# Kernel optimization log

Hardware: AMD Instinct MI355X
Metric: run time of the kernel (lower is better)

Reference implementation:

```python
import jax, jax.numpy as jnp
import numpy as np

B, S, H, W, L = 16, 2048, 512, 4, 2  # batch, seq, projection_dim, width, n_layers
EPS = 1e-5


def _ln(x, g, b):
    m = jnp.mean(x, axis=-1, keepdims=True)
    v = jnp.mean((x - m) ** 2, axis=-1, keepdims=True)
    return g * (x - m) * jax.lax.rsqrt(v + EPS) + b


def setup_inputs() -> dict:
    key = jax.random.key(0)
    ks = jax.random.split(key, 24)
    s = 0.02
    d = {
        'inputs': jax.random.normal(ks[0], (B, S, H), jnp.float32),
        'left_padding': jax.random.normal(ks[1], (W, H), jnp.float32) * s,
        'right_padding': jax.random.normal(ks[2], (W, H), jnp.float32) * s,
        'Wl': jax.random.normal(ks[3], (W * H, H), jnp.float32) * s,
        'bl': jnp.zeros((H,), jnp.float32),
        'Wr': jax.random.normal(ks[4], (W * H, H), jnp.float32) * s,
        'br': jnp.zeros((H,), jnp.float32),
        'lw1': jax.random.normal(ks[5], (L, H, H), jnp.float32) * s,
        'lb1': jnp.zeros((L, H), jnp.float32),
        'lw2': jax.random.normal(ks[6], (L, H, H), jnp.float32) * s,
        'lb2': jnp.zeros((L, H), jnp.float32),
        'lg': jnp.ones((L, H), jnp.float32),
        'lbeta': jnp.zeros((L, H), jnp.float32),
        'rw1': jax.random.normal(ks[7], (L, H, H), jnp.float32) * s,
        'rb1': jnp.zeros((L, H), jnp.float32),
        'rw2': jax.random.normal(ks[8], (L, H, H), jnp.float32) * s,
        'rb2': jnp.zeros((L, H), jnp.float32),
        'rg': jnp.ones((L, H), jnp.float32),
        'rbeta': jnp.zeros((L, H), jnp.float32),
    }
    return d


def reference(inputs, left_padding, right_padding, Wl, bl, Wr, br,
              lw1, lb1, lw2, lb2, lg, lbeta,
              rw1, rb1, rw2, rb2, rg, rbeta):
    b, s, h = inputs.shape
    w = left_padding.shape[0]
    padded = jnp.concatenate([
        jnp.broadcast_to(left_padding, (b, w, h)), inputs,
        jnp.broadcast_to(right_padding, (b, w, h))], axis=1)  # [B, W+S+W, H]
    t = jnp.arange(s)[:, None]
    off = jnp.arange(w)[None, :]
    left = padded[:, t + off].reshape(b, s, w * h)           # rows [t, t+w)
    right = padded[:, t + (w + 1) + off].reshape(b, s, w * h)  # rows [t+w+1, t+2w+1)
    lo = jax.nn.relu(jnp.einsum('bsk,kh->bsh', left, Wl) + bl)
    ro = jax.nn.relu(jnp.einsum('bsk,kh->bsh', right, Wr) + br)
    layers = []
    for i in range(lw1.shape[0]):
        # SublayerConnection: x + FF(LayerNorm(x)); FF = w2(relu(w1(.)))
        lo = lo + jnp.einsum('bsh,hk->bsk', jax.nn.relu(
            jnp.einsum('bsh,hk->bsk', _ln(lo, lg[i], lbeta[i]), lw1[i]) + lb1[i]), lw2[i]) + lb2[i]
        ro = ro + jnp.einsum('bsh,hk->bsk', jax.nn.relu(
            jnp.einsum('bsh,hk->bsk', _ln(ro, rg[i], rbeta[i]), rw1[i]) + rb1[i]), rw2[i]) + rb2[i]
        layers.append(jnp.concatenate([lo, ro], axis=-1))  # [B,S,2H]
    stacked = jnp.stack(layers, axis=0)                 # [L,B,S,2H]
    all_layers = jnp.transpose(stacked, (0, 2, 1, 3))   # [L,S,B,2H]
    last_layers = layers[-1]                            # [B,S,2H]
    return all_layers, last_layers
```

## Files before the change

### kernel.cpp

```cpp
#include <hip/hip_runtime.h>
#include <stdint.h>

#define Bx   16
#define Sx   2048
#define Hx   512
#define Lx   2
#define PHx  2056
#define Mx   32768

typedef float f32x4  __attribute__((ext_vector_type(4)));
typedef __bf16 bf16x8 __attribute__((ext_vector_type(8)));
typedef unsigned short u16x8 __attribute__((ext_vector_type(8)));

typedef __attribute__((address_space(1))) void gvoid_t;
typedef __attribute__((address_space(3))) void lvoid_t;

__device__ __forceinline__ unsigned short f2bf(float f) {
  uint32_t u = __float_as_uint(f);
  u += 0x7FFFu + ((u >> 16) & 1u);
  return (unsigned short)(u >> 16);
}

__global__ __launch_bounds__(256) void build_padded_k(
    const float* __restrict__ inp, const float* __restrict__ lp,
    const float* __restrict__ rp, unsigned short* __restrict__ padded) {
  int64_t idx = ((int64_t)blockIdx.x * 256 + threadIdx.x) * 8;
  int h = (int)(idx & 511);
  int64_t rowi = idx >> 9;
  int r = (int)(rowi % 2056);
  int b = (int)(rowi / 2056);
  const float* src;
  if (r < 4)          src = lp + r * 512 + h;
  else if (r < 2052)  src = inp + ((int64_t)b * 2048 + (r - 4)) * 512 + h;
  else                src = rp + (r - 2052) * 512 + h;
  float4 u = ((const float4*)src)[0];
  float4 w = ((const float4*)src)[1];
  u16x8 o;
  o[0] = f2bf(u.x); o[1] = f2bf(u.y); o[2] = f2bf(u.z); o[3] = f2bf(u.w);
  o[4] = f2bf(w.x); o[5] = f2bf(w.y); o[6] = f2bf(w.z); o[7] = f2bf(w.w);
  *(u16x8*)(padded + idx) = o;
}

__global__ __launch_bounds__(256) void prep_weights_k(
    const float* __restrict__ Wl, const float* __restrict__ Wr,
    const float* __restrict__ lw1, const float* __restrict__ lw2,
    const float* __restrict__ rw1, const float* __restrict__ rw2,
    unsigned short* __restrict__ Wlt, unsigned short* __restrict__ Wrt,
    unsigned short* __restrict__ lw1t, unsigned short* __restrict__ lw2t,
    unsigned short* __restrict__ rw1t, unsigned short* __restrict__ rw2t) {
  __shared__ unsigned short tl[32][36];
  int b = blockIdx.x;
  const float* src; unsigned short* dst; int K, tk, tn;
  if (b < 2048) {
    src = (b < 1024) ? Wl : Wr;
    dst = (b < 1024) ? Wlt : Wrt;
    int t = b & 1023; tk = t >> 4; tn = t & 15; K = 2048;
  } else {
    int b2 = b - 2048;
    int mat = b2 >> 8;
    const float* srcs[8] = {lw1, lw1 + 262144, lw2, lw2 + 262144,
                            rw1, rw1 + 262144, rw2, rw2 + 262144};
    unsigned short* dsts[8] = {lw1t, lw1t + 262144, lw2t, lw2t + 262144,
                               rw1t, rw1t + 262144, rw2t, rw2t + 262144};
    src = srcs[mat]; dst = dsts[mat];
    int tt = b2 & 255; tk = tt >> 4; tn = tt & 15; K = 512;
  }
  int t = threadIdx.x;
  int rr = t >> 3, c4 = (t & 7) * 4;
  float4 v = *(const float4*)(src + (int64_t)(tk * 32 + rr) * 512 + tn * 32 + c4);
  tl[c4 + 0][rr] = f2bf(v.x);
  tl[c4 + 1][rr] = f2bf(v.y);
  tl[c4 + 2][rr] = f2bf(v.z);
  tl[c4 + 3][rr] = f2bf(v.w);
  __syncthreads();
  int nn = t >> 3, k4 = (t & 7) * 4;
  ushort4 o = {tl[nn][k4], tl[nn][k4 + 1], tl[nn][k4 + 2], tl[nn][k4 + 3]};
  *(ushort4*)(dst + (int64_t)(tn * 32 + nn) * K + tk * 32 + k4) = o;
}

template <int MODE, bool STATS>
__global__ __launch_bounds__(256) void gemm_k(
    const unsigned short* __restrict__ A0, const unsigned short* __restrict__ A1,
    int64_t a_bstride, int a_off_per_z, int K,
    const unsigned short* __restrict__ Bt0, const unsigned short* __restrict__ Bt1,
    const float* __restrict__ bias0, const float* __restrict__ bias1,
    float* __restrict__ C, float* __restrict__ out0p, float* __restrict__ P) {
  __shared__ unsigned short sA[128 * 32];
  __shared__ unsigned short sB[128 * 32];
  __shared__ float sls[128][2][2];
  const int tid  = threadIdx.x;
  const int lane = tid & 63;
  const int wave = tid >> 6;
  const int m0 = blockIdx.x * 128;
  const int n0 = blockIdx.y * 128;
  const int z  = blockIdx.z;
  const int wm = (wave >> 1) * 64;
  const int wn = (wave & 1) * 64;
  const int fr = lane >> 4;
  const int fc = lane & 15;

  const unsigned short* A  = z ? A1 : A0;
  const unsigned short* Bt = z ? Bt1 : Bt0;
  const float* bias = z ? bias1 : bias0;
  const int a_off = z * a_off_per_z;
  const int c_off = z * 512;

  const unsigned short* Ablk =
      A + (int64_t)(m0 >> 11) * a_bstride + (int64_t)(m0 & 2047) * 512 + a_off;
  const unsigned short* Bblk = Bt + (int64_t)n0 * K;

  f32x4 acc[4][4] = {};

  const int t0 = tid, t1 = tid + 256;
  const int ar0 = t0 >> 2, ac0 = (t0 & 3) * 8;
  const int ar1 = t1 >> 2, ac1 = (t1 & 3) * 8;

  for (int k0 = 0; k0 < K; k0 += 32) {
    __builtin_amdgcn_global_load_lds(
        (gvoid_t*)(Ablk + (int64_t)ar0 * 512 + k0 + ac0),
        (lvoid_t*)(sA + t0 * 8), 16, 0, 0);
    __builtin_amdgcn_global_load_lds(
        (gvoid_t*)(Ablk + (int64_t)ar1 * 512 + k0 + ac1),
        (lvoid_t*)(sA + t1 * 8), 16, 0, 0);
    __builtin_amdgcn_global_load_lds(
        (gvoid_t*)(Bblk + (int64_t)ar0 * K + k0 + ac0),
        (lvoid_t*)(sB + t0 * 8), 16, 0, 0);
    __builtin_amdgcn_global_load_lds(
        (gvoid_t*)(Bblk + (int64_t)ar1 * K + k0 + ac1),
        (lvoid_t*)(sB + t1 * 8), 16, 0, 0);
    __syncthreads();

    bf16x8 af[4], bf[4];
#pragma unroll
    for (int i = 0; i < 4; i++)
      af[i] = *(const bf16x8*)(sA + (wm + i * 16 + fc) * 32 + fr * 8);
#pragma unroll
    for (int j = 0; j < 4; j++)
      bf[j] = *(const bf16x8*)(sB + (wn + j * 16 + fc) * 32 + fr * 8);
#pragma unroll
    for (int i = 0; i < 4; i++)
#pragma unroll
      for (int j = 0; j < 4; j++)
        acc[i][j] = __builtin_amdgcn_mfma_f32_16x16x32_bf16(af[i], bf[j], acc[i][j], 0, 0, 0);
    __syncthreads();
  }

  int col[4];
  float bv[4];
#pragma unroll
  for (int j = 0; j < 4; j++) {
    col[j] = n0 + wn + j * 16 + fc;
    bv[j] = bias[col[j]];
  }
  const int b_idx = m0 >> 11;
#pragma unroll
  for (int i = 0; i < 4; i++) {
#pragma unroll
    for (int r = 0; r < 4; r++) {
      const int m = m0 + wm + i * 16 + fr * 4 + r;
      const int64_t base = (int64_t)m * 1024 + c_off;
      float vs[4];
      if (MODE == 0) {
#pragma unroll
        for (int j = 0; j < 4; j++) {
          float v = acc[i][j][r] + bv[j];
          v = v > 0.f ? v : 0.f;
          C[base + col[j]] = v;
          vs[j] = v;
        }
      } else {
        const int s = m & 2047;
        const int64_t obase = (int64_t)s * 16384 + (int64_t)b_idx * 1024 + c_off;
#pragma unroll
        for (int j = 0; j < 4; j++) {
          float v = C[base + col[j]] + acc[i][j][r] + bv[j];
          C[base + col[j]] = v;
          out0p[obase + col[j]] = v;
          vs[j] = v;
        }
      }
      if (STATS) {
        float s1 = vs[0] + vs[1] + vs[2] + vs[3];
        float s2 = vs[0] * vs[0] + vs[1] * vs[1] + vs[2] * vs[2] + vs[3] * vs[3];
#pragma unroll
        for (int o = 1; o < 16; o <<= 1) {
          s1 += __shfl_xor(s1, o);
          s2 += __shfl_xor(s2, o);
        }
        if (fc == 0) {
          int li = (wave >> 1) * 64 + i * 16 + fr * 4 + r;
          sls[li][wave & 1][0] = s1;
          sls[li][wave & 1][1] = s2;
        }
      }
    }
  }
  if (STATS) {
    __syncthreads();
    int li = tid >> 1, comp = tid & 1;
    float v = sls[li][0][comp] + sls[li][1][comp];
    P[(((int64_t)z * 4 + blockIdx.y) * Mx + m0 + li) * 2 + comp] = v;
  }
}

__global__ __launch_bounds__(256) void gemm_ln_k(
    const float* __restrict__ state, const float* __restrict__ P,
    const float* __restrict__ g0, const float* __restrict__ g1p,
    const float* __restrict__ be0, const float* __restrict__ be1,
    const unsigned short* __restrict__ Bt0, const unsigned short* __restrict__ Bt1,
    const float* __restrict__ bias0, const float* __restrict__ bias1,
    unsigned short* __restrict__ hidden) {
  __shared__ unsigned short sA[128 * 32];
  __shared__ unsigned short sB[128 * 32];
  const int tid  = threadIdx.x;
  const int lane = tid & 63;
  const int wave = tid >> 6;
  const int m0 = blockIdx.x * 128;
  const int n0 = blockIdx.y * 128;
  const int z  = blockIdx.z;
  const int wm = (wave >> 1) * 64;
  const int wn = (wave & 1) * 64;
  const int fr = lane >> 4;
  const int fc = lane & 15;

  const unsigned short* Bt = z ? Bt1 : Bt0;
  const float* bias = z ? bias1 : bias0;
  const float* g    = z ? g1p : g0;
  const float* be   = z ? be1 : be0;
  const int c_off = z * 512;
  const unsigned short* Bblk = Bt + (int64_t)n0 * 512;

  const int row  = tid >> 1;
  const int half = tid & 1;
  const int m = m0 + row;
  const float* srcrow = state + (int64_t)m * 1024 + c_off + half * 16;

  float s1 = 0.f, s2 = 0.f;
#pragma unroll
  for (int nb = 0; nb < 4; nb++) {
    s1 += P[(((int64_t)z * 4 + nb) * Mx + m) * 2 + 0];
    s2 += P[(((int64_t)z * 4 + nb) * Mx + m) * 2 + 1];
  }
  const float mean = s1 * (1.0f / 512.0f);
  const float rstd = rsqrtf(s2 * (1.0f / 512.0f) - mean * mean + 1e-5f);

  f32x4 acc[4][4] = {};

  const int t0 = tid, t1 = tid + 256;
  const int br0 = t0 >> 2, bc0 = (t0 & 3) * 8;
  const int br1 = t1 >> 2, bc1 = (t1 & 3) * 8;

  for (int k0 = 0; k0 < 512; k0 += 32) {
    __builtin_amdgcn_global_load_lds(
        (gvoid_t*)(Bblk + (int64_t)br0 * 512 + k0 + bc0),
        (lvoid_t*)(sB + t0 * 8), 16, 0, 0);
    __builtin_amdgcn_global_load_lds(
        (gvoid_t*)(Bblk + (int64_t)br1 * 512 + k0 + bc1),
        (lvoid_t*)(sB + t1 * 8), 16, 0, 0);

    const float* sp = srcrow + k0;
    float xs[16], gs[16], bs[16];
    *(float4*)(xs + 0)  = ((const float4*)sp)[0];
    *(float4*)(xs + 4)  = ((const float4*)sp)[1];
    *(float4*)(xs + 8)  = ((const float4*)sp)[2];
    *(float4*)(xs + 12) = ((const float4*)sp)[3];
    const float* gp = g + k0 + half * 16;
    const float* bp = be + k0 + half * 16;
    *(float4*)(gs + 0)  = ((const float4*)gp)[0];
    *(float4*)(gs + 4)  = ((const float4*)gp)[1];
    *(float4*)(gs + 8)  = ((const float4*)gp)[2];
    *(float4*)(gs + 12) = ((const float4*)gp)[3];
    *(float4*)(bs + 0)  = ((const float4*)bp)[0];
    *(float4*)(bs + 4)  = ((const float4*)bp)[1];
    *(float4*)(bs + 8)  = ((const float4*)bp)[2];
    *(float4*)(bs + 12) = ((const float4*)bp)[3];
    u16x8 o0, o1;
#pragma unroll
    for (int t = 0; t < 8; t++)
      o0[t] = f2bf((xs[t] - mean) * rstd * gs[t] + bs[t]);
#pragma unroll
    for (int t = 0; t < 8; t++)
      o1[t] = f2bf((xs[t + 8] - mean) * rstd * gs[t + 8] + bs[t + 8]);
    *(u16x8*)(sA + row * 32 + half * 16)     = o0;
    *(u16x8*)(sA + row * 32 + half * 16 + 8) = o1;
    __syncthreads();

    bf16x8 af[4], bf[4];
#pragma unroll
    for (int i = 0; i < 4; i++)
      af[i] = *(const bf16x8*)(sA + (wm + i * 16 + fc) * 32 + fr * 8);
#pragma unroll
    for (int j = 0; j < 4; j++)
      bf[j] = *(const bf16x8*)(sB + (wn + j * 16 + fc) * 32 + fr * 8);
#pragma unroll
    for (int i = 0; i < 4; i++)
#pragma unroll
      for (int j = 0; j < 4; j++)
        acc[i][j] = __builtin_amdgcn_mfma_f32_16x16x32_bf16(af[i], bf[j], acc[i][j], 0, 0, 0);
    __syncthreads();
  }

  unsigned short* Cb = hidden + (int64_t)z * Mx * 512;
  int col[4];
  float bv[4];
#pragma unroll
  for (int j = 0; j < 4; j++) {
    col[j] = n0 + wn + j * 16 + fc;
    bv[j] = bias[col[j]];
  }
#pragma unroll
  for (int i = 0; i < 4; i++) {
#pragma unroll
    for (int r = 0; r < 4; r++) {
      const int mm = m0 + wm + i * 16 + fr * 4 + r;
      const int64_t base = (int64_t)mm * 512;
#pragma unroll
      for (int j = 0; j < 4; j++) {
        float v = acc[i][j][r] + bv[j];
        Cb[base + col[j]] = f2bf(v > 0.f ? v : 0.f);
      }
    }
  }
}

extern "C" void kernel_launch(void* const* d_in, const int* in_sizes, int n_in,
                              void* d_out, int out_size, void* d_ws, size_t ws_size,
                              hipStream_t stream) {
  const float* inputs = (const float*)d_in[0];
  const float* lp     = (const float*)d_in[1];
  const float* rp     = (const float*)d_in[2];
  const float* Wl     = (const float*)d_in[3];
  const float* bl     = (const float*)d_in[4];
  const float* Wr     = (const float*)d_in[5];
  const float* br     = (const float*)d_in[6];
  const float* lw1    = (const float*)d_in[7];
  const float* lb1    = (const float*)d_in[8];
  const float* lw2    = (const float*)d_in[9];
  const float* lb2    = (const float*)d_in[10];
  const float* lg     = (const float*)d_in[11];
  const float* lbeta  = (const float*)d_in[12];
  const float* rw1    = (const float*)d_in[13];
  const float* rb1    = (const float*)d_in[14];
  const float* rw2    = (const float*)d_in[15];
  const float* rb2    = (const float*)d_in[16];
  const float* rg     = (const float*)d_in[17];
  const float* rbeta  = (const float*)d_in[18];

  float* out0 = (float*)d_out;
  float* out1 = out0 + (int64_t)Lx * Sx * Bx * 1024;

  char* w = (char*)d_ws;
  auto take = [&](size_t n) { char* p = w; w += (n + 255) & ~(size_t)255; return p; };
  unsigned short* padded = (unsigned short*)take((size_t)Bx * PHx * Hx * 2);
  unsigned short* Wlt    = (unsigned short*)take(2048ull * 512 * 2);
  unsigned short* Wrt    = (unsigned short*)take(2048ull * 512 * 2);
  unsigned short* lw1t   = (unsigned short*)take((size_t)Lx * 512 * 512 * 2);
  unsigned short* lw2t   = (unsigned short*)take((size_t)Lx * 512 * 512 * 2);
  unsigned short* rw1t   = (unsigned short*)take((size_t)Lx * 512 * 512 * 2);
  unsigned short* rw2t   = (unsigned short*)take((size_t)Lx * 512 * 512 * 2);
  unsigned short* hidden = (unsigned short*)take((size_t)2 * Mx * 512 * 2);
  float*          Pst    = (float*)take((size_t)2 * 4 * Mx * 2 * 4);

  build_padded_k<<<8224, 256, 0, stream>>>(inputs, lp, rp, padded);
  prep_weights_k<<<4096, 256, 0, stream>>>(Wl, Wr, lw1, lw2, rw1, rw2,
                                           Wlt, Wrt, lw1t, lw2t, rw1t, rw2t);

  dim3 gg(256, 4, 2);
  gemm_k<0, true><<<gg, 256, 0, stream>>>(
      padded, padded, (int64_t)PHx * 512, 5 * 512, 2048,
      Wlt, Wrt, bl, br, out1, nullptr, Pst);

  for (int i = 0; i < Lx; i++) {
    gemm_ln_k<<<gg, 256, 0, stream>>>(
        out1, Pst, lg + i * 512, rg + i * 512, lbeta + i * 512, rbeta + i * 512,
        lw1t + (int64_t)i * 262144, rw1t + (int64_t)i * 262144,
        lb1 + i * 512, rb1 + i * 512, hidden);
    if (i == 0) {
      gemm_k<2, true><<<gg, 256, 0, stream>>>(
          hidden, hidden + (int64_t)Mx * 512, (int64_t)2048 * 512, 0, 512,
          lw2t, rw2t, lb2, rb2, out1, out0, Pst);
    } else {
      gemm_k<2, false><<<gg, 256, 0, stream>>>(
          hidden, hidden + (int64_t)Mx * 512, (int64_t)2048 * 512, 0, 512,
          lw2t + (int64_t)i * 262144, rw2t + (int64_t)i * 262144,
          lb2 + i * 512, rb2 + i * 512, out1,
          out0 + (int64_t)i * Sx * Bx * 1024, nullptr);
    }
  }
}
```

Baseline: 1.079 ms.

## Double K-tile depth to 64 and XOR-swizzle LDS layout in GEMM kernels

Both GEMM kernels now stage 64-wide K slices per iteration instead of 32, halving the number of barrier pairs per K loop. The LDS layout uses an XOR swizzle on 8-element chunks (applied on the global-load source address and on fragment reads) to avoid bank conflicts with the wider 128-byte rows. LDS use per block doubles, which may reduce occupancy.

```diff
diff --git a/kernel.cpp b/kernel.cpp
--- a/kernel.cpp
+++ b/kernel.cpp
@@ -20,6 +20,7 @@
   u += 0x7FFFu + ((u >> 16) & 1u);
   return (unsigned short)(u >> 16);
 }
+
 
 __global__ __launch_bounds__(256) void build_padded_k(
     const float* __restrict__ inp, const float* __restrict__ lp,
@@ -85,8 +86,8 @@
     const unsigned short* __restrict__ Bt0, const unsigned short* __restrict__ Bt1,
     const float* __restrict__ bias0, const float* __restrict__ bias1,
     float* __restrict__ C, float* __restrict__ out0p, float* __restrict__ P) {
-  __shared__ unsigned short sA[128 * 32];
-  __shared__ unsigned short sB[128 * 32];
+  __shared__ unsigned short sA[128 * 64];
+  __shared__ unsigned short sB[128 * 64];
   __shared__ float sls[128][2][2];
   const int tid  = threadIdx.x;
   const int lane = tid & 63;
@@ -98,6 +99,7 @@
   const int wn = (wave & 1) * 64;
   const int fr = lane >> 4;
   const int fc = lane & 15;
+  const int swf = (fc & 7) << 3;
 
   const unsigned short* A  = z ? A1 : A0;
   const unsigned short* Bt = z ? Bt1 : Bt0;
@@ -111,37 +113,37 @@
 
   f32x4 acc[4][4] = {};
 
-  const int t0 = tid, t1 = tid + 256;
-  const int ar0 = t0 >> 2, ac0 = (t0 & 3) * 8;
-  const int ar1 = t1 >> 2, ac1 = (t1 & 3) * 8;
-
-  for (int k0 = 0; k0 < K; k0 += 32) {
-    __builtin_amdgcn_global_load_lds(
-        (gvoid_t*)(Ablk + (int64_t)ar0 * 512 + k0 + ac0),
-        (lvoid_t*)(sA + t0 * 8), 16, 0, 0);
-    __builtin_amdgcn_global_load_lds(
-        (gvoid_t*)(Ablk + (int64_t)ar1 * 512 + k0 + ac1),
-        (lvoid_t*)(sA + t1 * 8), 16, 0, 0);
-    __builtin_amdgcn_global_load_lds(
-        (gvoid_t*)(Bblk + (int64_t)ar0 * K + k0 + ac0),
-        (lvoid_t*)(sB + t0 * 8), 16, 0, 0);
-    __builtin_amdgcn_global_load_lds(
-        (gvoid_t*)(Bblk + (int64_t)ar1 * K + k0 + ac1),
-        (lvoid_t*)(sB + t1 * 8), 16, 0, 0);
+  for (int k0 = 0; k0 < K; k0 += 64) {
+#pragma unroll
+    for (int r = 0; r < 4; r++) {
+      const int tt = tid + r * 256;
+      const int ar = tt >> 3;
+      const int ac = (tt & 7) * 8;
+      const int acs = ac ^ ((ar & 7) << 3);
+      __builtin_amdgcn_global_load_lds(
+          (gvoid_t*)(Ablk + (int64_t)ar * 512 + k0 + acs),
+          (lvoid_t*)(sA + tt * 8), 16, 0, 0);
+      __builtin_amdgcn_global_load_lds(
+          (gvoid_t*)(Bblk + (int64_t)ar * K + k0 + acs),
+          (lvoid_t*)(sB + tt * 8), 16, 0, 0);
+    }
     __syncthreads();
 
-    bf16x8 af[4], bf[4];
-#pragma unroll
-    for (int i = 0; i < 4; i++)
-      af[i] = *(const bf16x8*)(sA + (wm + i * 16 + fc) * 32 + fr * 8);
-#pragma unroll
-    for (int j = 0; j < 4; j++)
-      bf[j] = *(const bf16x8*)(sB + (wn + j * 16 + fc) * 32 + fr * 8);
-#pragma unroll
-    for (int i = 0; i < 4; i++)
+#pragma unroll
+    for (int kk = 0; kk < 2; kk++) {
+      bf16x8 af[4], bf[4];
+#pragma unroll
+      for (int i = 0; i < 4; i++)
+        af[i] = *(const bf16x8*)(sA + (((wm + i * 16 + fc) * 64 + kk * 32 + fr * 8) ^ swf));
 #pragma unroll
       for (int j = 0; j < 4; j++)
-        acc[i][j] = __builtin_amdgcn_mfma_f32_16x16x32_bf16(af[i], bf[j], acc[i][j], 0, 0, 0);
+        bf[j] = *(const bf16x8*)(sB + (((wn + j * 16 + fc) * 64 + kk * 32 + fr * 8) ^ swf));
+#pragma unroll
+      for (int i = 0; i < 4; i++)
+#pragma unroll
+        for (int j = 0; j < 4; j++)
+          acc[i][j] = __builtin_amdgcn_mfma_f32_16x16x32_bf16(af[i], bf[j], acc[i][j], 0, 0, 0);
+    }
     __syncthreads();
   }
 
@@ -210,8 +212,8 @@
     const unsigned short* __restrict__ Bt0, const unsigned short* __restrict__ Bt1,
     const float* __restrict__ bias0, const float* __restrict__ bias1,
     unsigned short* __restrict__ hidden) {
-  __shared__ unsigned short sA[128 * 32];
-  __shared__ unsigned short sB[128 * 32];
+  __shared__ unsigned short sA[128 * 64];
+  __shared__ unsigned short sB[128 * 64];
   const int tid  = threadIdx.x;
   const int lane = tid & 63;
   const int wave = tid >> 6;
@@ -222,6 +224,7 @@
   const int wn = (wave & 1) * 64;
   const int fr = lane >> 4;
   const int fc = lane & 15;
+  const int swf = (fc & 7) << 3;
 
   const unsigned short* Bt = z ? Bt1 : Bt0;
   const float* bias = z ? bias1 : bias0;
@@ -233,7 +236,8 @@
   const int row  = tid >> 1;
   const int half = tid & 1;
   const int m = m0 + row;
-  const float* srcrow = state + (int64_t)m * 1024 + c_off + half * 16;
+  const int swr = (row & 7) << 3;
+  const float* srcrow = state + (int64_t)m * 1024 + c_off;
 
   float s1 = 0.f, s2 = 0.f;
 #pragma unroll
@@ -246,57 +250,64 @@
 
   f32x4 acc[4][4] = {};
 
-  const int t0 = tid, t1 = tid + 256;
-  const int br0 = t0 >> 2, bc0 = (t0 & 3) * 8;
-  const int br1 = t1 >> 2, bc1 = (t1 & 3) * 8;
-
-  for (int k0 = 0; k0 < 512; k0 += 32) {
-    __builtin_amdgcn_global_load_lds(
-        (gvoid_t*)(Bblk + (int64_t)br0 * 512 + k0 + bc0),
-        (lvoid_t*)(sB + t0 * 8), 16, 0, 0);
-    __builtin_amdgcn_global_load_lds(
-        (gvoid_t*)(Bblk + (int64_t)br1 * 512 + k0 + bc1),
-        (lvoid_t*)(sB + t1 * 8), 16, 0, 0);
-
-    const float* sp = srcrow + k0;
-    float xs[16], gs[16], bs[16];
-    *(float4*)(xs + 0)  = ((const float4*)sp)[0];
-    *(float4*)(xs + 4)  = ((const float4*)sp)[1];
-    *(float4*)(xs + 8)  = ((const float4*)sp)[2];
-    *(float4*)(xs + 12) = ((const float4*)sp)[3];
-    const float* gp = g + k0 + half * 16;
-    const float* bp = be + k0 + half * 16;
-    *(float4*)(gs + 0)  = ((const float4*)gp)[0];
-    *(float4*)(gs + 4)  = ((const float4*)gp)[1];
-    *(float4*)(gs + 8)  = ((const float4*)gp)[2];
-    *(float4*)(gs + 12) = ((const float4*)gp)[3];
-    *(float4*)(bs + 0)  = ((const float4*)bp)[0];
-    *(float4*)(bs + 4)  = ((const float4*)bp)[1];
-    *(float4*)(bs + 8)  = ((const float4*)bp)[2];
-    *(float4*)(bs + 12) = ((const float4*)bp)[3];
-    u16x8 o0, o1;
-#pragma unroll
-    for (int t = 0; t < 8; t++)
-      o0[t] = f2bf((xs[t] - mean) * rstd * gs[t] + bs[t]);
-#pragma unroll
-    for (int t = 0; t < 8; t++)
-      o1[t] = f2bf((xs[t + 8] - mean) * rstd * gs[t + 8] + bs[t + 8]);
-    *(u16x8*)(sA + row * 32 + half * 16)     = o0;
-    *(u16x8*)(sA + row * 32 + half * 16 + 8) = o1;
+  for (int k0 = 0; k0 < 512; k0 += 64) {
+#pragma unroll
+    for (int r = 0; r < 4; r++) {
+      const int tt = tid + r * 256;
+      const int br = tt >> 3;
+      const int bc = (tt & 7) * 8;
+      const int bcs = bc ^ ((br & 7) << 3);
+      __builtin_amdgcn_global_load_lds(
+          (gvoid_t*)(Bblk + (int64_t)br * 512 + k0 + bcs),
+          (lvoid_t*)(sB + tt * 8), 16, 0, 0);
+    }
+
+#pragma unroll
+    for (int sc = 0; sc < 2; sc++) {
+      const int cb = half * 32 + sc * 16;
+      const float* xp = srcrow + k0 + cb;
+      const float* gp = g + k0 + cb;
+      const float* bp = be + k0 + cb;
+      float xs[16], gs[16], bs[16];
+      *(float4*)(xs + 0)  = ((const float4*)xp)[0];
+      *(float4*)(xs + 4)  = ((const float4*)xp)[1];
+      *(float4*)(xs + 8)  = ((const float4*)xp)[2];
+      *(float4*)(xs + 12) = ((const float4*)xp)[3];
+      *(float4*)(gs + 0)  = ((const float4*)gp)[0];
+      *(float4*)(gs + 4)  = ((const float4*)gp)[1];
+      *(float4*)(gs + 8)  = ((const float4*)gp)[2];
+      *(float4*)(gs + 12) = ((const float4*)gp)[3];
+      *(float4*)(bs + 0)  = ((const float4*)bp)[0];
+      *(float4*)(bs + 4)  = ((const float4*)bp)[1];
+      *(float4*)(bs + 8)  = ((const float4*)bp)[2];
+      *(float4*)(bs + 12) = ((const float4*)bp)[3];
+      u16x8 o0, o1;
+#pragma unroll
+      for (int t = 0; t < 8; t++)
+        o0[t] = f2bf((xs[t] - mean) * rstd * gs[t] + bs[t]);
+#pragma unroll
+      for (int t = 0; t < 8; t++)
+        o1[t] = f2bf((xs[t + 8] - mean) * rstd * gs[t + 8] + bs[t + 8]);
+      *(u16x8*)(sA + ((row * 64 + cb) ^ swr))     = o0;
+      *(u16x8*)(sA + ((row * 64 + cb + 8) ^ swr)) = o1;
+    }
     __syncthreads();
 
-    bf16x8 af[4], bf[4];
-#pragma unroll
-    for (int i = 0; i < 4; i++)
-      af[i] = *(const bf16x8*)(sA + (wm + i * 16 + fc) * 32 + fr * 8);
-#pragma unroll
-    for (int j = 0; j < 4; j++)
-      bf[j] = *(const bf16x8*)(sB + (wn + j * 16 + fc) * 32 + fr * 8);
-#pragma unroll
-    for (int i = 0; i < 4; i++)
+#pragma unroll
+    for (int kk = 0; kk < 2; kk++) {
+      bf16x8 af[4], bf[4];
+#pragma unroll
+      for (int i = 0; i < 4; i++)
+        af[i] = *(const bf16x8*)(sA + (((wm + i * 16 + fc) * 64 + kk * 32 + fr * 8) ^ swf));
 #pragma unroll
       for (int j = 0; j < 4; j++)
-        acc[i][j] = __builtin_amdgcn_mfma_f32_16x16x32_bf16(af[i], bf[j], acc[i][j], 0, 0, 0);
+        bf[j] = *(const bf16x8*)(sB + (((wn + j * 16 + fc) * 64 + kk * 32 + fr * 8) ^ swf));
+#pragma unroll
+      for (int i = 0; i < 4; i++)
+#pragma unroll
+        for (int j = 0; j < 4; j++)
+          acc[i][j] = __builtin_amdgcn_mfma_f32_16x16x32_bf16(af[i], bf[j], acc[i][j], 0, 0, 0);
+    }
     __syncthreads();
   }
 
```

After: 1.171 ms. 1.09x slower.

## Add 256x256-tile pipelined projection GEMM kernel with direct-to-LDS loads

Applied to the files above, without the earlier changes.

Replaces the generic 128x128 gemm_k used for the initial windowed projection (K=2048) with a dedicated 512-thread kernel. Each block computes a 256x256 output tile. The kernel uses global_load_lds async copies into eight swizzled LDS slots and hand-scheduled vmcnt waits and barriers, so loads overlap with MFMA work. It also raises wave priority around the MFMA bursts. The larger tile improves data reuse and cuts global traffic for the dominant GEMM, at the cost of 128KB of LDS, heavy register pressure and fragile manual scheduling.

```diff
diff --git a/kernel.cpp b/kernel.cpp
--- a/kernel.cpp
+++ b/kernel.cpp
@@ -20,6 +20,17 @@
   u += 0x7FFFu + ((u >> 16) & 1u);
   return (unsigned short)(u >> 16);
 }
+
+__device__ __forceinline__ void sbar() {
+  __builtin_amdgcn_sched_barrier(0);
+  __builtin_amdgcn_s_barrier();
+  __builtin_amdgcn_sched_barrier(0);
+}
+#define VMCNT(n) do {                                        \
+    __builtin_amdgcn_sched_barrier(0);                       \
+    asm volatile("s_waitcnt vmcnt(" #n ")" ::: "memory");    \
+    __builtin_amdgcn_sched_barrier(0);                       \
+  } while (0)
 
 __global__ __launch_bounds__(256) void build_padded_k(
     const float* __restrict__ inp, const float* __restrict__ lp,
@@ -78,6 +89,170 @@
   *(ushort4*)(dst + (int64_t)(tn * 32 + nn) * K + tk * 32 + k4) = o;
 }
 
+__global__ __launch_bounds__(512, 2) void proj8_k(
+    const unsigned short* __restrict__ A,
+    const unsigned short* __restrict__ Bt0, const unsigned short* __restrict__ Bt1,
+    const float* __restrict__ bias0, const float* __restrict__ bias1,
+    float* __restrict__ C, float* __restrict__ P) {
+  __shared__ unsigned short lds[8][8192];
+  const int tid  = threadIdx.x;
+  const int lane = tid & 63;
+  const int wave = tid >> 6;
+  const int wy = wave >> 2;
+  const int wx = wave & 3;
+  const int fr = lane >> 4;
+  const int fc = lane & 15;
+  const int m0   = blockIdx.x * 256;
+  const int nblk = blockIdx.y;
+  const int z    = blockIdx.z;
+
+  const unsigned short* Bt = z ? Bt1 : Bt0;
+  const float* bias = z ? bias1 : bias0;
+  const unsigned short* Ablk = A + (int64_t)(m0 >> 11) * ((int64_t)PHx * 512)
+                                 + (int64_t)(m0 & 2047) * 512 + z * 2560;
+  const unsigned short* Bblk = Bt + (int64_t)nblk * 256 * 2048;
+
+  auto stage = [&](int slot, int isB, int h, int tile) {
+#pragma unroll
+    for (int L = 0; L < 2; ++L) {
+      const int tt = tid + L * 512;
+      const int row = tt >> 3;
+      const int chunk = (tt & 7) * 8;
+      const int scol = chunk ^ (((row >> 2) & 1) << 4);
+      const unsigned short* src = isB
+          ? Bblk + (int64_t)(h * 128 + row) * 2048 + tile * 64 + scol
+          : Ablk + (int64_t)(h * 128 + row) * 512  + tile * 64 + scol;
+      __builtin_amdgcn_global_load_lds((gvoid_t*)src,
+          (lvoid_t*)(&lds[slot][tt * 8]), 16, 0, 0);
+    }
+  };
+  auto rdA = [&](int buf, int h, int i, int kk) -> bf16x8 {
+    const int row = wy * 64 + i * 16 + fc;
+    const int e = (row * 64 + kk * 32 + fr * 8) ^ (((row >> 2) & 1) << 4);
+    return *(const bf16x8*)(&lds[buf * 4 + h][e]);
+  };
+  auto rdB = [&](int buf, int h, int j, int kk) -> bf16x8 {
+    const int row = wx * 32 + j * 16 + fc;
+    const int e = (row * 64 + kk * 32 + fr * 8) ^ (((row >> 2) & 1) << 4);
+    return *(const bf16x8*)(&lds[buf * 4 + 2 + h][e]);
+  };
+
+  f32x4 acc[4][4][2] = {};
+
+  stage(0, 0, 0, 0);
+  stage(2, 1, 0, 0);
+  stage(1, 0, 1, 0);
+  stage(3, 1, 1, 0);
+  stage(4, 0, 0, 1);
+  stage(6, 1, 0, 1);
+  VMCNT(4);
+  sbar();
+
+  for (int t = 0; t < 16; ++t) {
+    const int t2 = 2 * t;
+    const bool notlast = (t < 15);
+#pragma unroll
+    for (int hv = 0; hv < 2; ++hv) {
+      const int buf = hv;
+#pragma unroll
+      for (int pp = 0; pp < 4; ++pp) {
+        const int mq = pp >> 1, nq = pp & 1;
+        bf16x8 af[4][2], bv[2][2];
+#pragma unroll
+        for (int i = 0; i < 4; ++i)
+#pragma unroll
+          for (int kk = 0; kk < 2; ++kk) af[i][kk] = rdA(buf, mq, i, kk);
+#pragma unroll
+        for (int j = 0; j < 2; ++j)
+#pragma unroll
+          for (int kk = 0; kk < 2; ++kk) bv[j][kk] = rdB(buf, nq, j, kk);
+
+        const int p = hv * 4 + pp;
+        if (p == 0)        stage(5, 0, 1, t2 + 1);
+        else if (p == 1)   stage(7, 1, 1, t2 + 1);
+        else if (notlast) {
+          if (p == 2)      stage(0, 0, 0, t2 + 2);
+          else if (p == 3) stage(2, 1, 0, t2 + 2);
+          else if (p == 4) stage(1, 0, 1, t2 + 2);
+          else if (p == 5) stage(3, 1, 1, t2 + 2);
+          else if (p == 6) stage(4, 0, 0, t2 + 3);
+          else             stage(6, 1, 0, t2 + 3);
+        }
+        sbar();
+        __builtin_amdgcn_s_setprio(1);
+#pragma unroll
+        for (int i = 0; i < 4; ++i)
+#pragma unroll
+          for (int j = 0; j < 2; ++j)
+#pragma unroll
+            for (int kk = 0; kk < 2; ++kk)
+              acc[pp][i][j] = __builtin_amdgcn_mfma_f32_16x16x32_bf16(
+                  af[i][kk], bv[j][kk], acc[pp][i][j], 0, 0, 0);
+        __builtin_amdgcn_s_setprio(0);
+        if (pp == 3) {
+          if (hv == 0) {
+            if (notlast) { VMCNT(4); } else { VMCNT(0); }
+          } else {
+            if (notlast) { VMCNT(4); }
+          }
+        }
+        sbar();
+      }
+    }
+  }
+
+  __syncthreads();
+
+  float* sls = (float*)&lds[0][0];
+  float bvv[2][2];
+#pragma unroll
+  for (int nq = 0; nq < 2; ++nq)
+#pragma unroll
+    for (int j = 0; j < 2; ++j)
+      bvv[nq][j] = bias[nblk * 256 + nq * 128 + wx * 32 + j * 16 + fc];
+
+#pragma unroll
+  for (int q = 0; q < 4; ++q) {
+    const int mq = q >> 1, nq = q & 1;
+#pragma unroll
+    for (int i = 0; i < 4; ++i) {
+#pragma unroll
+      for (int r = 0; r < 4; ++r) {
+        const int row_l = mq * 128 + wy * 64 + i * 16 + fr * 4 + r;
+        const int m = m0 + row_l;
+        float v0 = acc[q][i][0][r] + bvv[nq][0]; v0 = v0 > 0.f ? v0 : 0.f;
+        float v1 = acc[q][i][1][r] + bvv[nq][1]; v1 = v1 > 0.f ? v1 : 0.f;
+        const int64_t cb = (int64_t)m * 1024 + z * 512
+                           + nblk * 256 + nq * 128 + wx * 32 + fc;
+        C[cb] = v0;
+        C[cb + 16] = v1;
+        float s1 = v0 + v1, s2 = v0 * v0 + v1 * v1;
+#pragma unroll
+        for (int o = 1; o < 16; o <<= 1) {
+          s1 += __shfl_xor(s1, o);
+          s2 += __shfl_xor(s2, o);
+        }
+        if (fc == 0) {
+          sls[(row_l * 4 + wx) * 4 + nq * 2 + 0] = s1;
+          sls[(row_l * 4 + wx) * 4 + nq * 2 + 1] = s2;
+        }
+      }
+    }
+  }
+  __syncthreads();
+  {
+    const int row = tid >> 1, comp = tid & 1;
+#pragma unroll
+    for (int nq = 0; nq < 2; ++nq) {
+      float v = 0.f;
+#pragma unroll
+      for (int wxx = 0; wxx < 4; ++wxx)
+        v += sls[(row * 4 + wxx) * 4 + nq * 2 + comp];
+      P[(((int64_t)z * 4 + nblk * 2 + nq) * Mx + m0 + row) * 2 + comp] = v;
+    }
+  }
+}
+
 template <int MODE, bool STATS>
 __global__ __launch_bounds__(256) void gemm_k(
     const unsigned short* __restrict__ A0, const unsigned short* __restrict__ A1,
@@ -365,22 +540,20 @@
   prep_weights_k<<<4096, 256, 0, stream>>>(Wl, Wr, lw1, lw2, rw1, rw2,
                                            Wlt, Wrt, lw1t, lw2t, rw1t, rw2t);
 
-  dim3 gg(256, 4, 2);
-  gemm_k<0, true><<<gg, 256, 0, stream>>>(
-      padded, padded, (int64_t)PHx * 512, 5 * 512, 2048,
-      Wlt, Wrt, bl, br, out1, nullptr, Pst);
+  proj8_k<<<dim3(128, 2, 2), 512, 0, stream>>>(
+      padded, Wlt, Wrt, bl, br, out1, Pst);
 
   for (int i = 0; i < Lx; i++) {
-    gemm_ln_k<<<gg, 256, 0, stream>>>(
+    gemm_ln_k<<<dim3(256, 4, 2), 256, 0, stream>>>(
         out1, Pst, lg + i * 512, rg + i * 512, lbeta + i * 512, rbeta + i * 512,
         lw1t + (int64_t)i * 262144, rw1t + (int64_t)i * 262144,
         lb1 + i * 512, rb1 + i * 512, hidden);
     if (i == 0) {
-      gemm_k<2, true><<<gg, 256, 0, stream>>>(
+      gemm_k<2, true><<<dim3(256, 4, 2), 256, 0, stream>>>(
           hidden, hidden + (int64_t)Mx * 512, (int64_t)2048 * 512, 0, 512,
           lw2t, rw2t, lb2, rb2, out1, out0, Pst);
     } else {
-      gemm_k<2, false><<<gg, 256, 0, stream>>>(
+      gemm_k<2, false><<<dim3(256, 4, 2), 256, 0, stream>>>(
           hidden, hidden + (int64_t)Mx * 512, (int64_t)2048 * 512, 0, 512,
           lw2t + (int64_t)i * 262144, rw2t + (int64_t)i * 262144,
           lb2 + i * 512, rb2 + i * 512, out1,
```

Measured after the change: 1.080 ms. Within noise of the previous version (+0.1%).

## Double-buffer LDS tiles with XOR swizzle and enlarge gemm_k tile to 256 rows

Applied to the files above, without the earlier changes.

Both GEMM kernels now prefetch the next K-slice into a second LDS buffer while the current one feeds the MFMAs, which removes one barrier per iteration and overlaps global loads with compute. LDS column groups are XOR-swizzled by row to reduce bank conflicts on fragment reads. gemm_k moves to 512 threads with a 256x128 tile and half as many blocks, giving more reuse of B per block. The cost is more LDS per block and fewer blocks, which can lower occupancy.

```diff
diff --git a/kernel.cpp b/kernel.cpp
--- a/kernel.cpp
+++ b/kernel.cpp
@@ -20,6 +20,7 @@
   u += 0x7FFFu + ((u >> 16) & 1u);
   return (unsigned short)(u >> 16);
 }
+
 
 __global__ __launch_bounds__(256) void build_padded_k(
     const float* __restrict__ inp, const float* __restrict__ lp,
@@ -79,15 +80,148 @@
 }
 
 template <int MODE, bool STATS>
-__global__ __launch_bounds__(256) void gemm_k(
+__global__ __launch_bounds__(512) void gemm_k(
     const unsigned short* __restrict__ A0, const unsigned short* __restrict__ A1,
     int64_t a_bstride, int a_off_per_z, int K,
     const unsigned short* __restrict__ Bt0, const unsigned short* __restrict__ Bt1,
     const float* __restrict__ bias0, const float* __restrict__ bias1,
     float* __restrict__ C, float* __restrict__ out0p, float* __restrict__ P) {
-  __shared__ unsigned short sA[128 * 32];
-  __shared__ unsigned short sB[128 * 32];
-  __shared__ float sls[128][2][2];
+  __shared__ unsigned short sA[2][256 * 32];
+  __shared__ unsigned short sB[2][128 * 32];
+  __shared__ float sls[256][2][2];
+  const int tid  = threadIdx.x;
+  const int lane = tid & 63;
+  const int wave = tid >> 6;
+  const int m0 = blockIdx.x * 256;
+  const int n0 = blockIdx.y * 128;
+  const int z  = blockIdx.z;
+  const int wm = (wave >> 1) * 64;
+  const int wn = (wave & 1) * 64;
+  const int fr = lane >> 4;
+  const int fc = lane & 15;
+  const int swA = ((fr ^ (fc & 3)) << 3);
+
+  const unsigned short* A  = z ? A1 : A0;
+  const unsigned short* Bt = z ? Bt1 : Bt0;
+  const float* bias = z ? bias1 : bias0;
+  const int a_off = z * a_off_per_z;
+  const int c_off = z * 512;
+
+  const unsigned short* Ablk =
+      A + (int64_t)(m0 >> 11) * a_bstride + (int64_t)(m0 & 2047) * 512 + a_off;
+  const unsigned short* Bblk = Bt + (int64_t)n0 * K;
+
+  f32x4 acc[4][4] = {};
+
+  auto stage = [&](int k0, int buf) {
+#pragma unroll
+    for (int L = 0; L < 2; ++L) {
+      const int id = tid + L * 512;
+      const int row = id >> 2, g = id & 3;
+      const int sc = (g ^ (row & 3)) * 8;
+      __builtin_amdgcn_global_load_lds(
+          (gvoid_t*)(Ablk + (int64_t)row * 512 + k0 + sc),
+          (lvoid_t*)(&sA[buf][id * 8]), 16, 0, 0);
+    }
+    {
+      const int row = tid >> 2, g = tid & 3;
+      const int sc = (g ^ (row & 3)) * 8;
+      __builtin_amdgcn_global_load_lds(
+          (gvoid_t*)(Bblk + (int64_t)row * K + k0 + sc),
+          (lvoid_t*)(&sB[buf][tid * 8]), 16, 0, 0);
+    }
+  };
+
+  stage(0, 0);
+  __syncthreads();
+
+  int buf = 0;
+  for (int k0 = 0; k0 < K; k0 += 32) {
+    if (k0 + 32 < K) stage(k0 + 32, buf ^ 1);
+
+    bf16x8 af[4], bf[4];
+#pragma unroll
+    for (int i = 0; i < 4; i++)
+      af[i] = *(const bf16x8*)(&sA[buf][(wm + i * 16 + fc) * 32 + swA]);
+#pragma unroll
+    for (int j = 0; j < 4; j++)
+      bf[j] = *(const bf16x8*)(&sB[buf][(wn + j * 16 + fc) * 32 + swA]);
+#pragma unroll
+    for (int i = 0; i < 4; i++)
+#pragma unroll
+      for (int j = 0; j < 4; j++)
+        acc[i][j] = __builtin_amdgcn_mfma_f32_16x16x32_bf16(af[i], bf[j], acc[i][j], 0, 0, 0);
+    __syncthreads();
+    buf ^= 1;
+  }
+
+  int col[4];
+  float bv[4];
+#pragma unroll
+  for (int j = 0; j < 4; j++) {
+    col[j] = n0 + wn + j * 16 + fc;
+    bv[j] = bias[col[j]];
+  }
+  const int b_idx = m0 >> 11;
+#pragma unroll
+  for (int i = 0; i < 4; i++) {
+#pragma unroll
+    for (int r = 0; r < 4; r++) {
+      const int m = m0 + wm + i * 16 + fr * 4 + r;
+      const int64_t base = (int64_t)m * 1024 + c_off;
+      float vs[4];
+      if (MODE == 0) {
+#pragma unroll
+        for (int j = 0; j < 4; j++) {
+          float v = acc[i][j][r] + bv[j];
+          v = v > 0.f ? v : 0.f;
+          C[base + col[j]] = v;
+          vs[j] = v;
+        }
+      } else {
+        const int s = m & 2047;
+        const int64_t obase = (int64_t)s * 16384 + (int64_t)b_idx * 1024 + c_off;
+#pragma unroll
+        for (int j = 0; j < 4; j++) {
+          float v = C[base + col[j]] + acc[i][j][r] + bv[j];
+          C[base + col[j]] = v;
+          out0p[obase + col[j]] = v;
+          vs[j] = v;
+        }
+      }
+      if (STATS) {
+        float s1 = vs[0] + vs[1] + vs[2] + vs[3];
+        float s2 = vs[0] * vs[0] + vs[1] * vs[1] + vs[2] * vs[2] + vs[3] * vs[3];
+#pragma unroll
+        for (int o = 1; o < 16; o <<= 1) {
+          s1 += __shfl_xor(s1, o);
+          s2 += __shfl_xor(s2, o);
+        }
+        if (fc == 0) {
+          int li = wm + i * 16 + fr * 4 + r;
+          sls[li][wave & 1][0] = s1;
+          sls[li][wave & 1][1] = s2;
+        }
+      }
+    }
+  }
+  if (STATS) {
+    __syncthreads();
+    int li = tid >> 1, comp = tid & 1;
+    float v = sls[li][0][comp] + sls[li][1][comp];
+    P[(((int64_t)z * 4 + blockIdx.y) * Mx + m0 + li) * 2 + comp] = v;
+  }
+}
+
+__global__ __launch_bounds__(256) void gemm_ln_k(
+    const float* __restrict__ state, const float* __restrict__ P,
+    const float* __restrict__ g0, const float* __restrict__ g1p,
+    const float* __restrict__ be0, const float* __restrict__ be1,
+    const unsigned short* __restrict__ Bt0, const unsigned short* __restrict__ Bt1,
+    const float* __restrict__ bias0, const float* __restrict__ bias1,
+    unsigned short* __restrict__ hidden) {
+  __shared__ unsigned short sA[2][128 * 32];
+  __shared__ unsigned short sB[2][128 * 32];
   const int tid  = threadIdx.x;
   const int lane = tid & 63;
   const int wave = tid >> 6;
@@ -98,130 +232,7 @@
   const int wn = (wave & 1) * 64;
   const int fr = lane >> 4;
   const int fc = lane & 15;
-
-  const unsigned short* A  = z ? A1 : A0;
-  const unsigned short* Bt = z ? Bt1 : Bt0;
-  const float* bias = z ? bias1 : bias0;
-  const int a_off = z * a_off_per_z;
-  const int c_off = z * 512;
-
-  const unsigned short* Ablk =
-      A + (int64_t)(m0 >> 11) * a_bstride + (int64_t)(m0 & 2047) * 512 + a_off;
-  const unsigned short* Bblk = Bt + (int64_t)n0 * K;
-
-  f32x4 acc[4][4] = {};
-
-  const int t0 = tid, t1 = tid + 256;
-  const int ar0 = t0 >> 2, ac0 = (t0 & 3) * 8;
-  const int ar1 = t1 >> 2, ac1 = (t1 & 3) * 8;
-
-  for (int k0 = 0; k0 < K; k0 += 32) {
-    __builtin_amdgcn_global_load_lds(
-        (gvoid_t*)(Ablk + (int64_t)ar0 * 512 + k0 + ac0),
-        (lvoid_t*)(sA + t0 * 8), 16, 0, 0);
-    __builtin_amdgcn_global_load_lds(
-        (gvoid_t*)(Ablk + (int64_t)ar1 * 512 + k0 + ac1),
-        (lvoid_t*)(sA + t1 * 8), 16, 0, 0);
-    __builtin_amdgcn_global_load_lds(
-        (gvoid_t*)(Bblk + (int64_t)ar0 * K + k0 + ac0),
-        (lvoid_t*)(sB + t0 * 8), 16, 0, 0);
-    __builtin_amdgcn_global_load_lds(
-        (gvoid_t*)(Bblk + (int64_t)ar1 * K + k0 + ac1),
-        (lvoid_t*)(sB + t1 * 8), 16, 0, 0);
-    __syncthreads();
-
-    bf16x8 af[4], bf[4];
-#pragma unroll
-    for (int i = 0; i < 4; i++)
-      af[i] = *(const bf16x8*)(sA + (wm + i * 16 + fc) * 32 + fr * 8);
-#pragma unroll
-    for (int j = 0; j < 4; j++)
-      bf[j] = *(const bf16x8*)(sB + (wn + j * 16 + fc) * 32 + fr * 8);
-#pragma unroll
-    for (int i = 0; i < 4; i++)
-#pragma unroll
-      for (int j = 0; j < 4; j++)
-        acc[i][j] = __builtin_amdgcn_mfma_f32_16x16x32_bf16(af[i], bf[j], acc[i][j], 0, 0, 0);
-    __syncthreads();
-  }
-
-  int col[4];
-  float bv[4];
-#pragma unroll
-  for (int j = 0; j < 4; j++) {
-    col[j] = n0 + wn + j * 16 + fc;
-    bv[j] = bias[col[j]];
-  }
-  const int b_idx = m0 >> 11;
-#pragma unroll
-  for (int i = 0; i < 4; i++) {
-#pragma unroll
-    for (int r = 0; r < 4; r++) {
-      const int m = m0 + wm + i * 16 + fr * 4 + r;
-      const int64_t base = (int64_t)m * 1024 + c_off;
-      float vs[4];
-      if (MODE == 0) {
-#pragma unroll
-        for (int j = 0; j < 4; j++) {
-          float v = acc[i][j][r] + bv[j];
-          v = v > 0.f ? v : 0.f;
-          C[base + col[j]] = v;
-          vs[j] = v;
-        }
-      } else {
-        const int s = m & 2047;
-        const int64_t obase = (int64_t)s * 16384 + (int64_t)b_idx * 1024 + c_off;
-#pragma unroll
-        for (int j = 0; j < 4; j++) {
-          float v = C[base + col[j]] + acc[i][j][r] + bv[j];
-          C[base + col[j]] = v;
-          out0p[obase + col[j]] = v;
-          vs[j] = v;
-        }
-      }
-      if (STATS) {
-        float s1 = vs[0] + vs[1] + vs[2] + vs[3];
-        float s2 = vs[0] * vs[0] + vs[1] * vs[1] + vs[2] * vs[2] + vs[3] * vs[3];
-#pragma unroll
-        for (int o = 1; o < 16; o <<= 1) {
-          s1 += __shfl_xor(s1, o);
-          s2 += __shfl_xor(s2, o);
-        }
-        if (fc == 0) {
-          int li = (wave >> 1) * 64 + i * 16 + fr * 4 + r;
-          sls[li][wave & 1][0] = s1;
-          sls[li][wave & 1][1] = s2;
-        }
-      }
-    }
-  }
-  if (STATS) {
-    __syncthreads();
-    int li = tid >> 1, comp = tid & 1;
-    float v = sls[li][0][comp] + sls[li][1][comp];
-    P[(((int64_t)z * 4 + blockIdx.y) * Mx + m0 + li) * 2 + comp] = v;
-  }
-}
-
-__global__ __launch_bounds__(256) void gemm_ln_k(
-    const float* __restrict__ state, const float* __restrict__ P,
-    const float* __restrict__ g0, const float* __restrict__ g1p,
-    const float* __restrict__ be0, const float* __restrict__ be1,
-    const unsigned short* __restrict__ Bt0, const unsigned short* __restrict__ Bt1,
-    const float* __restrict__ bias0, const float* __restrict__ bias1,
-    unsigned short* __restrict__ hidden) {
-  __shared__ unsigned short sA[128 * 32];
-  __shared__ unsigned short sB[128 * 32];
-  const int tid  = threadIdx.x;
-  const int lane = tid & 63;
-  const int wave = tid >> 6;
-  const int m0 = blockIdx.x * 128;
-  const int n0 = blockIdx.y * 128;
-  const int z  = blockIdx.z;
-  const int wm = (wave >> 1) * 64;
-  const int wn = (wave & 1) * 64;
-  const int fr = lane >> 4;
-  const int fc = lane & 15;
+  const int swA = ((fr ^ (fc & 3)) << 3);
 
   const unsigned short* Bt = z ? Bt1 : Bt0;
   const float* bias = z ? bias1 : bias0;
@@ -234,6 +245,8 @@
   const int half = tid & 1;
   const int m = m0 + row;
   const float* srcrow = state + (int64_t)m * 1024 + c_off + half * 16;
+  const int d0 = row * 32 + (((half * 2 + 0) ^ (row & 3)) << 3);
+  const int d1 = row * 32 + (((half * 2 + 1) ^ (row & 3)) << 3);
 
   float s1 = 0.f, s2 = 0.f;
 #pragma unroll
@@ -244,60 +257,65 @@
   const float mean = s1 * (1.0f / 512.0f);
   const float rstd = rsqrtf(s2 * (1.0f / 512.0f) - mean * mean + 1e-5f);
 
-  f32x4 acc[4][4] = {};
-
-  const int t0 = tid, t1 = tid + 256;
-  const int br0 = t0 >> 2, bc0 = (t0 & 3) * 8;
-  const int br1 = t1 >> 2, bc1 = (t1 & 3) * 8;
-
-  for (int k0 = 0; k0 < 512; k0 += 32) {
-    __builtin_amdgcn_global_load_lds(
-        (gvoid_t*)(Bblk + (int64_t)br0 * 512 + k0 + bc0),
-        (lvoid_t*)(sB + t0 * 8), 16, 0, 0);
-    __builtin_amdgcn_global_load_lds(
-        (gvoid_t*)(Bblk + (int64_t)br1 * 512 + k0 + bc1),
-        (lvoid_t*)(sB + t1 * 8), 16, 0, 0);
-
+  auto stageB = [&](int k0, int buf) {
+#pragma unroll
+    for (int L = 0; L < 2; ++L) {
+      const int id = tid + L * 256;
+      const int br = id >> 2, bg = id & 3;
+      const int sc = (bg ^ (br & 3)) * 8;
+      __builtin_amdgcn_global_load_lds(
+          (gvoid_t*)(Bblk + (int64_t)br * 512 + k0 + sc),
+          (lvoid_t*)(&sB[buf][id * 8]), 16, 0, 0);
+    }
+  };
+  auto stageA = [&](int k0, int buf) {
     const float* sp = srcrow + k0;
-    float xs[16], gs[16], bs[16];
-    *(float4*)(xs + 0)  = ((const float4*)sp)[0];
-    *(float4*)(xs + 4)  = ((const float4*)sp)[1];
-    *(float4*)(xs + 8)  = ((const float4*)sp)[2];
-    *(float4*)(xs + 12) = ((const float4*)sp)[3];
     const float* gp = g + k0 + half * 16;
     const float* bp = be + k0 + half * 16;
-    *(float4*)(gs + 0)  = ((const float4*)gp)[0];
-    *(float4*)(gs + 4)  = ((const float4*)gp)[1];
-    *(float4*)(gs + 8)  = ((const float4*)gp)[2];
-    *(float4*)(gs + 12) = ((const float4*)gp)[3];
-    *(float4*)(bs + 0)  = ((const float4*)bp)[0];
-    *(float4*)(bs + 4)  = ((const float4*)bp)[1];
-    *(float4*)(bs + 8)  = ((const float4*)bp)[2];
-    *(float4*)(bs + 12) = ((const float4*)bp)[3];
-    u16x8 o0, o1;
-#pragma unroll
-    for (int t = 0; t < 8; t++)
-      o0[t] = f2bf((xs[t] - mean) * rstd * gs[t] + bs[t]);
-#pragma unroll
-    for (int t = 0; t < 8; t++)
-      o1[t] = f2bf((xs[t + 8] - mean) * rstd * gs[t + 8] + bs[t + 8]);
-    *(u16x8*)(sA + row * 32 + half * 16)     = o0;
-    *(u16x8*)(sA + row * 32 + half * 16 + 8) = o1;
-    __syncthreads();
+#pragma unroll
+    for (int c = 0; c < 2; ++c) {
+      float xs[8], gs[8], bs[8];
+      *(float4*)(xs + 0) = ((const float4*)sp)[c * 2 + 0];
+      *(float4*)(xs + 4) = ((const float4*)sp)[c * 2 + 1];
+      *(float4*)(gs + 0) = ((const float4*)gp)[c * 2 + 0];
+      *(float4*)(gs + 4) = ((const float4*)gp)[c * 2 + 1];
+      *(float4*)(bs + 0) = ((const float4*)bp)[c * 2 + 0];
+      *(float4*)(bs + 4) = ((const float4*)bp)[c * 2 + 1];
+      u16x8 o;
+#pragma unroll
+      for (int t = 0; t < 8; t++)
+        o[t] = f2bf((xs[t] - mean) * rstd * gs[t] + bs[t]);
+      *(u16x8*)(&sA[buf][c == 0 ? d0 : d1]) = o;
+    }
+  };
+
+  f32x4 acc[4][4] = {};
+
+  stageB(0, 0);
+  stageA(0, 0);
+  __syncthreads();
+
+  int buf = 0;
+  for (int k0 = 0; k0 < 512; k0 += 32) {
+    if (k0 + 32 < 512) {
+      stageB(k0 + 32, buf ^ 1);
+      stageA(k0 + 32, buf ^ 1);
+    }
 
     bf16x8 af[4], bf[4];
 #pragma unroll
     for (int i = 0; i < 4; i++)
-      af[i] = *(const bf16x8*)(sA + (wm + i * 16 + fc) * 32 + fr * 8);
+      af[i] = *(const bf16x8*)(&sA[buf][(wm + i * 16 + fc) * 32 + swA]);
 #pragma unroll
     for (int j = 0; j < 4; j++)
-      bf[j] = *(const bf16x8*)(sB + (wn + j * 16 + fc) * 32 + fr * 8);
+      bf[j] = *(const bf16x8*)(&sB[buf][(wn + j * 16 + fc) * 32 + swA]);
 #pragma unroll
     for (int i = 0; i < 4; i++)
 #pragma unroll
       for (int j = 0; j < 4; j++)
         acc[i][j] = __builtin_amdgcn_mfma_f32_16x16x32_bf16(af[i], bf[j], acc[i][j], 0, 0, 0);
     __syncthreads();
+    buf ^= 1;
   }
 
   unsigned short* Cb = hidden + (int64_t)z * Mx * 512;
@@ -365,22 +383,21 @@
   prep_weights_k<<<4096, 256, 0, stream>>>(Wl, Wr, lw1, lw2, rw1, rw2,
                                            Wlt, Wrt, lw1t, lw2t, rw1t, rw2t);
 
-  dim3 gg(256, 4, 2);
-  gemm_k<0, true><<<gg, 256, 0, stream>>>(
+  gemm_k<0, true><<<dim3(128, 4, 2), 512, 0, stream>>>(
       padded, padded, (int64_t)PHx * 512, 5 * 512, 2048,
       Wlt, Wrt, bl, br, out1, nullptr, Pst);
 
   for (int i = 0; i < Lx; i++) {
-    gemm_ln_k<<<gg, 256, 0, stream>>>(
+    gemm_ln_k<<<dim3(256, 4, 2), 256, 0, stream>>>(
         out1, Pst, lg + i * 512, rg + i * 512, lbeta + i * 512, rbeta + i * 512,
         lw1t + (int64_t)i * 262144, rw1t + (int64_t)i * 262144,
         lb1 + i * 512, rb1 + i * 512, hidden);
     if (i == 0) {
-      gemm_k<2, true><<<gg, 256, 0, stream>>>(
+      gemm_k<2, true><<<dim3(128, 4, 2), 512, 0, stream>>>(
           hidden, hidden + (int64_t)Mx * 512, (int64_t)2048 * 512, 0, 512,
           lw2t, rw2t, lb2, rb2, out1, out0, Pst);
     } else {
-      gemm_k<2, false><<<gg, 256, 0, stream>>>(
+      gemm_k<2, false><<<dim3(128, 4, 2), 512, 0, stream>>>(
           hidden, hidden + (int64_t)Mx * 512, (int64_t)2048 * 512, 0, 512,
           lw2t + (int64_t)i * 262144, rw2t + (int64_t)i * 262144,
           lb2 + i * 512, rb2 + i * 512, out1,
```

New measurement: 1.011 ms. 6.3% less time.
